# Performance work log

Hardware: AMD Instinct MI355X
Metric: run time of the kernel (lower is better)

Reference implementation:

```python
import jax, jax.numpy as jnp
import numpy as np
import math

N_HEAD = 16
HEAD_DIM = 64
LN_EPS = 1e-5
TEMP = 1.0

def _layernorm(x, scale, bias):
    # normalize over last dim (head_dim)
    mu = jnp.mean(x, axis=-1, keepdims=True)
    var = jnp.mean(jnp.square(x - mu), axis=-1, keepdims=True)
    return (x - mu) / jnp.sqrt(var + LN_EPS) * scale + bias

def setup_inputs() -> dict:
    key = jax.random.key(0)
    ks = jax.random.split(key, 3)
    B, S, C = 4, 2048, 1024
    x = jax.random.normal(ks[0], (B, S, C), dtype=jnp.float32)
    w_qkv = jax.random.normal(ks[1], (C, 3 * C), dtype=jnp.float32) * (C ** -0.5)
    w_proj = jax.random.normal(ks[2], (C, C), dtype=jnp.float32) * (C ** -0.5)
    return {
        "x": x,
        "w_qkv": w_qkv,
        "w_proj": w_proj,
        "q_scale": jnp.ones((HEAD_DIM,), jnp.float32),
        "q_bias": jnp.zeros((HEAD_DIM,), jnp.float32),
        "k_scale": jnp.ones((HEAD_DIM,), jnp.float32),
        "k_bias": jnp.zeros((HEAD_DIM,), jnp.float32),
    }

def reference(x, w_qkv, w_proj, q_scale, q_bias, k_scale, k_bias):
    B, S, C = x.shape
    H, D = N_HEAD, HEAD_DIM
    # qkv projection -> [B,S,3,H,D] -> [3,B,H,S,D]
    qkv = (x @ w_qkv).reshape(B, S, 3, H, D).transpose(2, 0, 3, 1, 4)
    q = _layernorm(qkv[0], q_scale, q_bias)
    k = _layernorm(qkv[1], k_scale, k_bias)
    v = qkv[2]
    # temperature-scaled logits, stable softmax
    inv = 1.0 / (math.sqrt(D) * max(TEMP, 1e-6))
    logits = jnp.einsum('bhqd,bhkd->bhqk', q, k) * inv
    att = jax.nn.softmax(logits, axis=-1)
    # entropy stats (track_stats=True path)
    s_raw = -jnp.sum(att * jnp.log(att + 1e-9), axis=-1)  # [B,H,S]
    batch_entropies = jnp.mean(s_raw / math.log(S), axis=(1, 2))  # [B]
    out = jnp.einsum('bhqk,bhkd->bhqd', att, v).transpose(0, 2, 1, 3).reshape(B, S, C)
    return out @ w_proj, batch_entropies
```

## Files before the change

### kernel.cpp

```cpp
#include <hip/hip_runtime.h>
#include <hip/hip_bf16.h>
#include <math.h>

#define CB 4
#define CS 2048
#define CC 1024
#define CH 16
#define CD 64
#define CBS (CB*CS)

typedef unsigned short u16;
typedef __bf16 bf16x8 __attribute__((ext_vector_type(8)));
typedef float f32x4 __attribute__((ext_vector_type(4)));
typedef float f32x16 __attribute__((ext_vector_type(16)));
typedef unsigned short u16x4 __attribute__((ext_vector_type(4)));
typedef unsigned short u16x8 __attribute__((ext_vector_type(8)));
typedef unsigned u32x2 __attribute__((ext_vector_type(2)));

__device__ __forceinline__ u16 f2bf(float f){
  union { float f; unsigned u; } v; v.f = f;
  unsigned r = v.u + 0x7FFFu + ((v.u >> 16) & 1u);
  return (u16)(r >> 16);
}
__device__ __forceinline__ unsigned pack2bf(float a, float b){
  __hip_bfloat162 h = __float22bfloat162_rn(make_float2(a, b));
  union { __hip_bfloat162 h; unsigned u; } c; c.h = h; return c.u;
}
__device__ __forceinline__ f32x4 mfma16(bf16x8 a, bf16x8 b, f32x4 c){
  return __builtin_amdgcn_mfma_f32_16x16x32_bf16(a, b, c, 0, 0, 0);
}
__device__ __forceinline__ f32x16 mfma32(bf16x8 a, bf16x8 b, f32x16 c){
  return __builtin_amdgcn_mfma_f32_32x32x16_bf16(a, b, c, 0, 0, 0);
}
__device__ __forceinline__ void gload16(const u16* g, u16* lds_base_uniform){
  __builtin_amdgcn_global_load_lds(
      (const __attribute__((address_space(1))) unsigned int*)g,
      (__attribute__((address_space(3))) unsigned int*)lds_base_uniform, 16, 0, 0);
}

__global__ __launch_bounds__(256) void convert_x_kernel(
    const float* __restrict__ x, u16* __restrict__ xb, float* __restrict__ zero4){
  if (blockIdx.x == 0 && threadIdx.x < 4) zero4[threadIdx.x] = 0.0f;
  size_t i = ((size_t)blockIdx.x*256 + threadIdx.x)*8;
  float4 a = *(const float4*)(x+i);
  float4 b = *(const float4*)(x+i+4);
  u16x8 o = { f2bf(a.x),f2bf(a.y),f2bf(a.z),f2bf(a.w),
              f2bf(b.x),f2bf(b.y),f2bf(b.z),f2bf(b.w) };
  *(u16x8*)(xb+i) = o;
}

template<int K, int N>
__global__ __launch_bounds__(256) void transpose_convert_kernel(
    const float* __restrict__ w, u16* __restrict__ wt){
  __shared__ u16 tile[64][65];
  const int nb = N/64;
  int tk0 = (blockIdx.x / nb) * 64;
  int tn0 = (blockIdx.x % nb) * 64;
  int t = threadIdx.x;
  for (int i = 0; i < 4; i++) {
    int r = i*16 + (t>>4);
    int c = (t&15)*4;
    float4 v = *(const float4*)(w + (size_t)(tk0+r)*N + tn0 + c);
    tile[c+0][r]=f2bf(v.x); tile[c+1][r]=f2bf(v.y);
    tile[c+2][r]=f2bf(v.z); tile[c+3][r]=f2bf(v.w);
  }
  __syncthreads();
  for (int i = 0; i < 4; i++) {
    int r = i*16 + (t>>4);
    int c = (t&15)*4;
    u16x4 o = { tile[r][c+0], tile[r][c+1], tile[r][c+2], tile[r][c+3] };
    *(u16x4*)(wt + (size_t)(tn0+r)*K + tk0 + c) = o;
  }
}

__global__ __launch_bounds__(256) void transpose_v_kernel(
    const u16* __restrict__ vb, u16* __restrict__ vtb){
  __shared__ u16 tile[64][72];
  int bh = blockIdx.x >> 5;
  int st = blockIdx.x & 31;
  int t = threadIdx.x;
  const u16* src = vb + (size_t)bh*CS*CD + (size_t)st*64*CD;
  int r = t>>2, c = (t&3)*16;
  *(u16x8*)&tile[r][c]   = *(const u16x8*)(src + (size_t)r*CD + c);
  *(u16x8*)&tile[r][c+8] = *(const u16x8*)(src + (size_t)r*CD + c + 8);
  __syncthreads();
  int d = t>>2, s = (t&3)*16;
  u16x8 o0, o1;
  for (int j=0;j<8;j++){ o0[j] = tile[s+j][d]; o1[j] = tile[s+8+j][d]; }
  u16* dst = vtb + (size_t)bh*CD*CS + (size_t)d*CS + st*64 + s;
  *(u16x8*)dst = o0;
  *(u16x8*)(dst+8) = o1;
}

__global__ __launch_bounds__(256, 2) void gemm_qkv_ln_kernel(
    const u16* __restrict__ xb, const u16* __restrict__ wqkvT,
    const float* __restrict__ qsc, const float* __restrict__ qbi,
    const float* __restrict__ ksc, const float* __restrict__ kbi,
    u16* __restrict__ qb, u16* __restrict__ kb, u16* __restrict__ vb){
  __shared__ __align__(16) u16 al[3][128*32];
  __shared__ __align__(16) u16 bl[3][128*32];
  int t = threadIdx.x;
  int wv = t >> 6, lane = t & 63, lo = lane & 15, q4 = lane >> 4;
  int m0 = blockIdx.x * 128;
  int n0 = blockIdx.y * 128;
  int lsA = (lane & 3) ^ ((lane >> 3) & 3);
  const u16* ag0 = xb    + (size_t)(m0 + (lane>>2))*CC + lsA*8;
  const u16* bg0 = wqkvT + (size_t)(n0 + (lane>>2))*CC + lsA*8;

  f32x4 acc[2][8];
  #pragma unroll
  for (int i=0;i<2;i++)
    #pragma unroll
    for (int j=0;j<8;j++) acc[i][j] = (f32x4){0.f,0.f,0.f,0.f};

  auto stage = [&](int buf, int kk){
    #pragma unroll
    for (int cc=0; cc<2; cc++){
      int c = wv*2 + cc;
      gload16(ag0 + (size_t)c*16*CC + kk*32, &al[buf][c*512]);
      gload16(bg0 + (size_t)c*16*CC + kk*32, &bl[buf][c*512]);
    }
  };

  stage(0, 0);
  stage(1, 1);
  int cur = 0;
  const int akey = (lo >> 1) & 3;

  for (int kk = 0; kk < 32; kk++){
    if (kk < 30){
      asm volatile("s_waitcnt vmcnt(4)" ::: "memory");
      __builtin_amdgcn_s_barrier();
      __builtin_amdgcn_sched_barrier(0);
      int nb = cur + 2; if (nb >= 3) nb -= 3;
      stage(nb, kk + 2);
    } else if (kk == 30){
      asm volatile("s_waitcnt vmcnt(4)" ::: "memory");
      __builtin_amdgcn_s_barrier();
      __builtin_amdgcn_sched_barrier(0);
    } else {
      asm volatile("s_waitcnt vmcnt(0)" ::: "memory");
      __builtin_amdgcn_s_barrier();
      __builtin_amdgcn_sched_barrier(0);
    }
    const u16* ac = &al[cur][0];
    const u16* bc = &bl[cur][0];
    int soff = (q4 ^ akey) << 3;
    bf16x8 a0 = *(const bf16x8*)&ac[(wv*32      + lo)*32 + soff];
    bf16x8 a1 = *(const bf16x8*)&ac[(wv*32 + 16 + lo)*32 + soff];
    __builtin_amdgcn_s_setprio(1);
    #pragma unroll
    for (int nt=0; nt<8; nt++){
      bf16x8 b = *(const bf16x8*)&bc[(nt*16 + lo)*32 + soff];
      acc[0][nt] = mfma16(a0, b, acc[0][nt]);
      acc[1][nt] = mfma16(a1, b, acc[1][nt]);
    }
    __builtin_amdgcn_s_setprio(0);
    cur = (cur == 2) ? 0 : cur + 1;
  }

  int three = n0 >> 10;
  int h0 = (n0 & 1023) >> 6;
  const float* scp = (three == 0) ? qsc : ksc;
  const float* bip = (three == 0) ? qbi : kbi;
  float outscale = (three == 0) ? 0.125f * 1.44269504088896f : 1.0f;
  u16* dst = (three == 0) ? qb : (three == 1 ? kb : vb);

  for (int rt = 0; rt < 2; rt++){
    int tg = m0 + wv*32 + rt*16 + q4*4;
    for (int hf = 0; hf < 2; hf++){
      int h = h0 + hf;
      for (int r = 0; r < 4; r++){
        int token = tg + r;
        int bb = token >> 11, ss = token & (CS-1);
        size_t base = (((size_t)(bb*CH + h))*CS + ss)*CD;
        if (three < 2){
          float s1 = 0.f, s2 = 0.f;
          for (int j=0;j<4;j++){ float v = acc[rt][hf*4+j][r]; s1 += v; s2 += v*v; }
          for (int off=8; off>=1; off>>=1){
            s1 += __shfl_xor(s1, off, 16);
            s2 += __shfl_xor(s2, off, 16);
          }
          float mean = s1 * (1.f/64.f);
          float var  = s2 * (1.f/64.f) - mean*mean;
          float rstd = rsqrtf(var + 1e-5f);
          for (int j=0;j<4;j++){
            int d = j*16 + lo;
            float v = (acc[rt][hf*4+j][r] - mean) * rstd * scp[d] + bip[d];
            dst[base + d] = f2bf(v * outscale);
          }
        } else {
          for (int j=0;j<4;j++){
            int d = j*16 + lo;
            dst[base + d] = f2bf(acc[rt][hf*4+j][r]);
          }
        }
      }
    }
  }
}

__global__ __launch_bounds__(256, 2) void attention_kernel(
    const u16* __restrict__ qb, const u16* __restrict__ kb,
    const u16* __restrict__ vtb, u16* __restrict__ attnb, float* __restrict__ ent){
  __shared__ __align__(16) u16 kl[3][32*64];
  __shared__ __align__(16) u16 vl[3][64*32];
  int t = threadIdx.x;
  int wv = t >> 6, lane = t & 63;
  int col = lane & 31, hi = lane >> 5;
  int n = blockIdx.x;
  int xc = n & 7, j = n >> 3;
  int bh = xc + 8*(j >> 4);
  int qt = j & 15;
  int bI = bh >> 4;
  int q0w = qt*128 + wv*32;
  const u16* qbp = qb  + (size_t)bh * CS * CD;
  const u16* kbp = kb  + (size_t)bh * CS * CD;
  const u16* vbp = vtb + (size_t)bh * CD * CS;

  int srow8  = lane >> 3, sl8 = lane & 7;
  int srow16 = lane >> 2, sl4 = lane & 3;

  bf16x8 qf[4];
  #pragma unroll
  for (int ks=0;ks<4;ks++)
    qf[ks] = *(const bf16x8*)(qbp + (size_t)(q0w + col)*CD + ks*16 + hi*8);

  f32x16 o[2];
  #pragma unroll
  for (int nt=0;nt<2;nt++)
    #pragma unroll
    for (int i=0;i<16;i++) o[nt][i] = 0.f;
  float zacc = 0.f, tacc = 0.f;

  auto stage = [&](int buf, int tile){
    int skn = tile*32;
    int krow  = wv*8 + srow8;
    int kslot = sl8 ^ srow8 ^ wv;
    gload16(kbp + (size_t)(skn + krow)*CD + kslot*8, &kl[buf][wv*512]);
    int vrow  = wv*16 + srow16;
    int vslot = sl4 ^ (srow16 & 3);
    gload16(vbp + (size_t)vrow*CS + skn + vslot*8, &vl[buf][wv*512]);
  };

  stage(0, 0);
  stage(1, 1);

  const int kkey = (col & 7) ^ (col >> 3);
  const int vkey = (col & 3);
  int cur = 0;

  for (int it = 0; it < 64; it++){
    if (it < 62){
      asm volatile("s_waitcnt vmcnt(2)" ::: "memory");
      __builtin_amdgcn_s_barrier();
      __builtin_amdgcn_sched_barrier(0);
      int nb = cur + 2; if (nb >= 3) nb -= 3;
      stage(nb, it + 2);
    } else if (it == 62){
      asm volatile("s_waitcnt vmcnt(2)" ::: "memory");
      __builtin_amdgcn_s_barrier();
      __builtin_amdgcn_sched_barrier(0);
    } else {
      asm volatile("s_waitcnt vmcnt(0)" ::: "memory");
      __builtin_amdgcn_s_barrier();
      __builtin_amdgcn_sched_barrier(0);
    }
    const u16* kc = &kl[cur][0];
    const u16* vc = &vl[cur][0];

    bf16x8 kfr[4], vfr[2][2];
    #pragma unroll
    for (int ks=0;ks<4;ks++)
      kfr[ks] = *(const bf16x8*)&kc[col*64 + (((2*ks+hi) ^ kkey)<<3)];
    #pragma unroll
    for (int nt=0;nt<2;nt++)
      #pragma unroll
      for (int ks=0;ks<2;ks++)
        vfr[nt][ks] = *(const bf16x8*)&vc[(nt*32+col)*32 + (((ks*2+hi) ^ vkey)<<3)];

    f32x16 sf;
    #pragma unroll
    for (int i=0;i<16;i++) sf[i] = 0.f;
    __builtin_amdgcn_s_setprio(1);
    #pragma unroll
    for (int ks=0;ks<4;ks++)
      sf = mfma32(kfr[ks], qf[ks], sf);
    __builtin_amdgcn_s_setprio(0);

    #pragma unroll
    for (int ksl=0; ksl<2; ksl++){
      float p[2][4];
      #pragma unroll
      for (int gg=0; gg<2; gg++){
        int g = 2*ksl + gg;
        float l0 = sf[g*4+0], l1 = sf[g*4+1],
              l2 = sf[g*4+2], l3 = sf[g*4+3];
        float p0 = __builtin_amdgcn_exp2f(l0);
        float p1 = __builtin_amdgcn_exp2f(l1);
        float p2 = __builtin_amdgcn_exp2f(l2);
        float p3 = __builtin_amdgcn_exp2f(l3);
        zacc += (p0+p1)+(p2+p3);
        tacc += (p0*l0+p1*l1)+(p2*l2+p3*l3);
        p[gg][0]=p0; p[gg][1]=p1; p[gg][2]=p2; p[gg][3]=p3;
      }
      unsigned x0 = pack2bf(p[0][0], p[0][1]);
      unsigned x1 = pack2bf(p[0][2], p[0][3]);
      unsigned y0 = pack2bf(p[1][0], p[1][1]);
      unsigned y1 = pack2bf(p[1][2], p[1][3]);
      u32x2 s0 = __builtin_amdgcn_permlane32_swap(x0, y0, false, false);
      u32x2 s1 = __builtin_amdgcn_permlane32_swap(x1, y1, false, false);
      union { unsigned u[4]; bf16x8 v; } ap;
      ap.u[0] = s0[0]; ap.u[1] = s1[0]; ap.u[2] = s0[1]; ap.u[3] = s1[1];
      __builtin_amdgcn_s_setprio(1);
      o[0] = mfma32(ap.v, vfr[0][ksl], o[0]);
      o[1] = mfma32(ap.v, vfr[1][ksl], o[1]);
      __builtin_amdgcn_s_setprio(0);
    }
    cur = (cur == 2) ? 0 : cur + 1;
  }

  float z2 = zacc + __shfl_xor(zacc, 32);
  float t2 = tacc + __shfl_xor(tacc, 32);
  float invz = 1.f / z2;

  float srowv = 0.69314718055995f * (__builtin_amdgcn_logf(z2) - t2 * invz);
  float ev = (hi == 0) ? srowv : 0.f;
  for (int off=1; off<=32; off<<=1) ev += __shfl_xor(ev, off);
  if (lane == 0){
    float entscale = 1.0f / ((float)CH * (float)CS * logf((float)CS));
    atomicAdd(&ent[bI], ev * entscale);
  }

  float izv[4][4];
  #pragma unroll
  for (int g=0; g<4; g++)
    #pragma unroll
    for (int r=0; r<4; r++)
      izv[g][r] = __shfl(invz, 8*g + 4*hi + r);

  u16* obase = attnb + ((size_t)bh*CS + q0w)*CD;
  #pragma unroll
  for (int nt=0;nt<2;nt++){
    #pragma unroll
    for (int g=0;g<4;g++){
      #pragma unroll
      for (int r=0;r<4;r++){
        int qrow = 8*g + 4*hi + r;
        obase[(size_t)qrow*CD + nt*32 + col] = f2bf(o[nt][g*4+r] * izv[g][r]);
      }
    }
  }
}

__global__ __launch_bounds__(256, 2) void gemm_out_kernel(
    const u16* __restrict__ attnH, const u16* __restrict__ wprojT,
    float* __restrict__ out){
  __shared__ __align__(16) u16 al[3][128*32];
  __shared__ __align__(16) u16 bl[3][128*32];
  int t = threadIdx.x;
  int wv = t >> 6, lane = t & 63, lo = lane & 15, q4 = lane >> 4;
  int m0 = blockIdx.x * 128;
  int n0 = blockIdx.y * 128;
  int b  = m0 >> 11, s0 = m0 & (CS-1);
  int lsA = (lane & 3) ^ ((lane >> 3) & 3);
  const u16* bg0 = wprojT + (size_t)(n0 + (lane>>2))*CC + lsA*8;

  f32x4 acc[2][8];
  #pragma unroll
  for (int i=0;i<2;i++)
    #pragma unroll
    for (int j=0;j<8;j++) acc[i][j] = (f32x4){0.f,0.f,0.f,0.f};

  auto stage = [&](int buf, int kk){
    int h = kk >> 1, doff = (kk & 1) * 32;
    #pragma unroll
    for (int cc=0; cc<2; cc++){
      int c = wv*2 + cc;
      gload16(attnH + ((size_t)(b*CH + h)*CS + s0 + c*16 + (lane>>2))*CD + doff + lsA*8,
              &al[buf][c*512]);
      gload16(bg0 + (size_t)c*16*CC + kk*32, &bl[buf][c*512]);
    }
  };

  stage(0, 0);
  stage(1, 1);
  int cur = 0;
  const int akey = (lo >> 1) & 3;

  for (int kk = 0; kk < 32; kk++){
    if (kk < 30){
      asm volatile("s_waitcnt vmcnt(4)" ::: "memory");
      __builtin_amdgcn_s_barrier();
      __builtin_amdgcn_sched_barrier(0);
      int nb = cur + 2; if (nb >= 3) nb -= 3;
      stage(nb, kk + 2);
    } else if (kk == 30){
      asm volatile("s_waitcnt vmcnt(4)" ::: "memory");
      __builtin_amdgcn_s_barrier();
      __builtin_amdgcn_sched_barrier(0);
    } else {
      asm volatile("s_waitcnt vmcnt(0)" ::: "memory");
      __builtin_amdgcn_s_barrier();
      __builtin_amdgcn_sched_barrier(0);
    }
    const u16* ac = &al[cur][0];
    const u16* bc = &bl[cur][0];
    int soff = (q4 ^ akey) << 3;
    bf16x8 a0 = *(const bf16x8*)&ac[(wv*32      + lo)*32 + soff];
    bf16x8 a1 = *(const bf16x8*)&ac[(wv*32 + 16 + lo)*32 + soff];
    __builtin_amdgcn_s_setprio(1);
    #pragma unroll
    for (int nt=0; nt<8; nt++){
      bf16x8 b2 = *(const bf16x8*)&bc[(nt*16 + lo)*32 + soff];
      acc[0][nt] = mfma16(a0, b2, acc[0][nt]);
      acc[1][nt] = mfma16(a1, b2, acc[1][nt]);
    }
    __builtin_amdgcn_s_setprio(0);
    cur = (cur == 2) ? 0 : cur + 1;
  }

  for (int rt=0;rt<2;rt++){
    for (int r=0;r<4;r++){
      int row = m0 + wv*32 + rt*16 + q4*4 + r;
      for (int nt=0;nt<8;nt++)
        out[(size_t)row*CC + n0 + nt*16 + lo] = acc[rt][nt][r];
    }
  }
}

extern "C" void kernel_launch(void* const* d_in, const int* in_sizes, int n_in,
                              void* d_out, int out_size, void* d_ws, size_t ws_size,
                              hipStream_t stream) {
  const float* x      = (const float*)d_in[0];
  const float* w_qkv  = (const float*)d_in[1];
  const float* w_proj = (const float*)d_in[2];
  const float* q_scale= (const float*)d_in[3];
  const float* q_bias = (const float*)d_in[4];
  const float* k_scale= (const float*)d_in[5];
  const float* k_bias = (const float*)d_in[6];
  float* out = (float*)d_out;
  float* ent = out + (size_t)CBS * CC;

  u16* xb     = (u16*)d_ws;
  u16* wqkvT  = xb     + (size_t)CBS*CC;
  u16* wprojT = wqkvT  + (size_t)3*CC*CC;
  u16* qb     = wprojT + (size_t)CC*CC;
  u16* kb     = qb + (size_t)CB*CH*CS*CD;
  u16* vb     = kb + (size_t)CB*CH*CS*CD;
  u16* vbT    = xb;
  u16* attn   = vb;

  convert_x_kernel<<<dim3(CBS*CC/(256*8)), 256, 0, stream>>>(x, xb, ent);
  transpose_convert_kernel<CC, 3*CC><<<dim3((CC/64)*(3*CC/64)), 256, 0, stream>>>(w_qkv, wqkvT);
  transpose_convert_kernel<CC, CC><<<dim3((CC/64)*(CC/64)), 256, 0, stream>>>(w_proj, wprojT);
  gemm_qkv_ln_kernel<<<dim3(CBS/128, 3*CC/128), 256, 0, stream>>>(
      xb, wqkvT, q_scale, q_bias, k_scale, k_bias, qb, kb, vb);
  transpose_v_kernel<<<dim3(CB*CH*(CS/64)), 256, 0, stream>>>(vb, vbT);
  attention_kernel<<<dim3(CB*CH*(CS/128)), 256, 0, stream>>>(qb, kb, vbT, attn, ent);
  gemm_out_kernel<<<dim3(CBS/128, CC/128), 256, 0, stream>>>(attn, wprojT, out);
}
```

Baseline: 335.3 us.

## Load GEMM A operand directly into registers, drop its LDS staging

In both the QKV and output-projection GEMMs, each wave now reads its own A rows straight from global memory into registers, one k-step ahead, instead of staging A through a triple-buffered LDS ring. This halves shared-memory use per block, and the launch bound is raised from 2 to 3 blocks per CU to use the freed space. The cost is that A latency is hidden by only one iteration of register prefetch. The plain global loads also add to the vmcnt counter that the hand-written waitcnt logic relies on, so the compiler may insert stricter waits. Per-lane A accesses are 16-byte pieces from separate rows, which are less coalesced than the previous async LDS loads.

```diff
diff --git a/kernel.cpp b/kernel.cpp
--- a/kernel.cpp
+++ b/kernel.cpp
@@ -92,20 +92,20 @@
   *(u16x8*)(dst+8) = o1;
 }
 
-__global__ __launch_bounds__(256, 2) void gemm_qkv_ln_kernel(
+__global__ __launch_bounds__(256, 3) void gemm_qkv_ln_kernel(
     const u16* __restrict__ xb, const u16* __restrict__ wqkvT,
     const float* __restrict__ qsc, const float* __restrict__ qbi,
     const float* __restrict__ ksc, const float* __restrict__ kbi,
     u16* __restrict__ qb, u16* __restrict__ kb, u16* __restrict__ vb){
-  __shared__ __align__(16) u16 al[3][128*32];
   __shared__ __align__(16) u16 bl[3][128*32];
   int t = threadIdx.x;
   int wv = t >> 6, lane = t & 63, lo = lane & 15, q4 = lane >> 4;
   int m0 = blockIdx.x * 128;
   int n0 = blockIdx.y * 128;
-  int lsA = (lane & 3) ^ ((lane >> 3) & 3);
-  const u16* ag0 = xb    + (size_t)(m0 + (lane>>2))*CC + lsA*8;
-  const u16* bg0 = wqkvT + (size_t)(n0 + (lane>>2))*CC + lsA*8;
+  int lsB = (lane & 3) ^ ((lane >> 3) & 3);
+  const u16* bg0  = wqkvT + (size_t)(n0 + (lane>>2))*CC + lsB*8;
+  const u16* agl0 = xb + (size_t)(m0 + wv*32 + lo)*CC + q4*8;
+  const u16* agl1 = agl0 + (size_t)16*CC;
 
   f32x4 acc[2][8];
   #pragma unroll
@@ -113,17 +113,18 @@
     #pragma unroll
     for (int j=0;j<8;j++) acc[i][j] = (f32x4){0.f,0.f,0.f,0.f};
 
-  auto stage = [&](int buf, int kk){
+  auto stageB = [&](int buf, int kk){
     #pragma unroll
     for (int cc=0; cc<2; cc++){
       int c = wv*2 + cc;
-      gload16(ag0 + (size_t)c*16*CC + kk*32, &al[buf][c*512]);
       gload16(bg0 + (size_t)c*16*CC + kk*32, &bl[buf][c*512]);
     }
   };
 
-  stage(0, 0);
-  stage(1, 1);
+  stageB(0, 0);
+  stageB(1, 1);
+  bf16x8 acur0 = *(const bf16x8*)(agl0);
+  bf16x8 acur1 = *(const bf16x8*)(agl1);
   int cur = 0;
   const int akey = (lo >> 1) & 3;
 
@@ -133,7 +134,7 @@
       __builtin_amdgcn_s_barrier();
       __builtin_amdgcn_sched_barrier(0);
       int nb = cur + 2; if (nb >= 3) nb -= 3;
-      stage(nb, kk + 2);
+      stageB(nb, kk + 2);
     } else if (kk == 30){
       asm volatile("s_waitcnt vmcnt(4)" ::: "memory");
       __builtin_amdgcn_s_barrier();
@@ -143,19 +144,24 @@
       __builtin_amdgcn_s_barrier();
       __builtin_amdgcn_sched_barrier(0);
     }
-    const u16* ac = &al[cur][0];
+    bf16x8 anxt0, anxt1;
+    if (kk < 31){
+      anxt0 = *(const bf16x8*)(agl0 + (kk+1)*32);
+      anxt1 = *(const bf16x8*)(agl1 + (kk+1)*32);
+    } else {
+      anxt0 = acur0; anxt1 = acur1;
+    }
     const u16* bc = &bl[cur][0];
     int soff = (q4 ^ akey) << 3;
-    bf16x8 a0 = *(const bf16x8*)&ac[(wv*32      + lo)*32 + soff];
-    bf16x8 a1 = *(const bf16x8*)&ac[(wv*32 + 16 + lo)*32 + soff];
     __builtin_amdgcn_s_setprio(1);
     #pragma unroll
     for (int nt=0; nt<8; nt++){
       bf16x8 b = *(const bf16x8*)&bc[(nt*16 + lo)*32 + soff];
-      acc[0][nt] = mfma16(a0, b, acc[0][nt]);
-      acc[1][nt] = mfma16(a1, b, acc[1][nt]);
+      acc[0][nt] = mfma16(acur0, b, acc[0][nt]);
+      acc[1][nt] = mfma16(acur1, b, acc[1][nt]);
     }
     __builtin_amdgcn_s_setprio(0);
+    acur0 = anxt0; acur1 = anxt1;
     cur = (cur == 2) ? 0 : cur + 1;
   }
 
@@ -353,18 +359,19 @@
   }
 }
 
-__global__ __launch_bounds__(256, 2) void gemm_out_kernel(
+__global__ __launch_bounds__(256, 3) void gemm_out_kernel(
     const u16* __restrict__ attnH, const u16* __restrict__ wprojT,
     float* __restrict__ out){
-  __shared__ __align__(16) u16 al[3][128*32];
   __shared__ __align__(16) u16 bl[3][128*32];
   int t = threadIdx.x;
   int wv = t >> 6, lane = t & 63, lo = lane & 15, q4 = lane >> 4;
   int m0 = blockIdx.x * 128;
   int n0 = blockIdx.y * 128;
   int b  = m0 >> 11, s0 = m0 & (CS-1);
-  int lsA = (lane & 3) ^ ((lane >> 3) & 3);
-  const u16* bg0 = wprojT + (size_t)(n0 + (lane>>2))*CC + lsA*8;
+  int lsB = (lane & 3) ^ ((lane >> 3) & 3);
+  const u16* bg0 = wprojT + (size_t)(n0 + (lane>>2))*CC + lsB*8;
+  const u16* agl0 = attnH + ((size_t)(b*CH)*CS + s0 + wv*32 + lo)*CD + q4*8;
+  const u16* agl1 = agl0 + (size_t)16*CD;
 
   f32x4 acc[2][8];
   #pragma unroll
@@ -372,19 +379,21 @@
     #pragma unroll
     for (int j=0;j<8;j++) acc[i][j] = (f32x4){0.f,0.f,0.f,0.f};
 
-  auto stage = [&](int buf, int kk){
-    int h = kk >> 1, doff = (kk & 1) * 32;
+  auto aoff = [&](int kk) -> size_t {
+    return (size_t)(kk >> 1)*CS*CD + (size_t)(kk & 1)*32;
+  };
+  auto stageB = [&](int buf, int kk){
     #pragma unroll
     for (int cc=0; cc<2; cc++){
       int c = wv*2 + cc;
-      gload16(attnH + ((size_t)(b*CH + h)*CS + s0 + c*16 + (lane>>2))*CD + doff + lsA*8,
-              &al[buf][c*512]);
       gload16(bg0 + (size_t)c*16*CC + kk*32, &bl[buf][c*512]);
     }
   };
 
-  stage(0, 0);
-  stage(1, 1);
+  stageB(0, 0);
+  stageB(1, 1);
+  bf16x8 acur0 = *(const bf16x8*)(agl0);
+  bf16x8 acur1 = *(const bf16x8*)(agl1);
   int cur = 0;
   const int akey = (lo >> 1) & 3;
 
@@ -394,7 +403,7 @@
       __builtin_amdgcn_s_barrier();
       __builtin_amdgcn_sched_barrier(0);
       int nb = cur + 2; if (nb >= 3) nb -= 3;
-      stage(nb, kk + 2);
+      stageB(nb, kk + 2);
     } else if (kk == 30){
       asm volatile("s_waitcnt vmcnt(4)" ::: "memory");
       __builtin_amdgcn_s_barrier();
@@ -404,19 +413,25 @@
       __builtin_amdgcn_s_barrier();
       __builtin_amdgcn_sched_barrier(0);
     }
-    const u16* ac = &al[cur][0];
+    bf16x8 anxt0, anxt1;
+    if (kk < 31){
+      size_t ao = aoff(kk + 1);
+      anxt0 = *(const bf16x8*)(agl0 + ao);
+      anxt1 = *(const bf16x8*)(agl1 + ao);
+    } else {
+      anxt0 = acur0; anxt1 = acur1;
+    }
     const u16* bc = &bl[cur][0];
     int soff = (q4 ^ akey) << 3;
-    bf16x8 a0 = *(const bf16x8*)&ac[(wv*32      + lo)*32 + soff];
-    bf16x8 a1 = *(const bf16x8*)&ac[(wv*32 + 16 + lo)*32 + soff];
     __builtin_amdgcn_s_setprio(1);
     #pragma unroll
     for (int nt=0; nt<8; nt++){
       bf16x8 b2 = *(const bf16x8*)&bc[(nt*16 + lo)*32 + soff];
-      acc[0][nt] = mfma16(a0, b2, acc[0][nt]);
-      acc[1][nt] = mfma16(a1, b2, acc[1][nt]);
+      acc[0][nt] = mfma16(acur0, b2, acc[0][nt]);
+      acc[1][nt] = mfma16(acur1, b2, acc[1][nt]);
     }
     __builtin_amdgcn_s_setprio(0);
+    acur0 = anxt0; acur1 = anxt1;
     cur = (cur == 2) ? 0 : cur + 1;
   }
 
```

Measured after the change: 332.8 us. About the same (-0.7%).
